# Performance work log

Hardware: AMD Instinct MI355X
Metric: run time of the kernel (lower is better)

The kernel has to match this reference:

```python
import jax, jax.numpy as jnp
import numpy as np

RADIUS = 0.3
NSAMPLE = 64
GROUPS = 8
GN_EPS = 1e-5
B, N = 8, 2048


def safe_norm(x, axis=-1, keepdims=False):
    # norm that matches sqrt exactly for nonzero inputs and returns 0 (not nan-grad) at 0
    ss = jnp.sum(x * x, axis=axis, keepdims=keepdims)
    zero = ss < 1e-20
    n = jnp.sqrt(jnp.where(zero, 1.0, ss))
    return jnp.where(zero, 0.0, n)


def angle(v1, v2):
    cross = jnp.cross(v1, v2)
    cn = jnp.sum(cross * cross, axis=-1)
    dot = jnp.sum(v1 * v2, axis=-1)
    deg = (cn < 1e-20) & (jnp.abs(dot) < 1e-12)
    cn_s = jnp.where(cn < 1e-20, 0.0, jnp.sqrt(jnp.where(cn < 1e-20, 1.0, cn)))
    ang = jnp.arctan2(cn_s, jnp.where(deg, 1.0, dot))
    return jnp.where(deg, 0.0, ang)  # torch atan2(0,0) = 0


def group_norm(x, gamma, beta):
    # x: [B, C, ...]; GroupNorm(8, C) over (C/8, spatial) per group
    b, c = x.shape[0], x.shape[1]
    xg = x.reshape(b, GROUPS, c // GROUPS, -1)
    mean = jnp.mean(xg, axis=(2, 3), keepdims=True)
    var = jnp.mean((xg - mean) ** 2, axis=(2, 3), keepdims=True)
    xn = ((xg - mean) * jax.lax.rsqrt(var + GN_EPS)).reshape(x.shape)
    bshape = (1, c) + (1,) * (x.ndim - 2)
    return xn * gamma.reshape(bshape) + beta.reshape(bshape)


def conv2d_1x1(x, w, b):  # x [B,Ci,S,N] -> [B,Co,S,N]
    return jnp.einsum('oc,bcsn->bosn', w, x) + b[None, :, None, None]


def conv1d_1x1(x, w, b):  # x [B,Ci,N] -> [B,Co,N]
    return jnp.einsum('oc,bcn->bon', w, x) + b[None, :, None]


def sample_and_group(xyz, normals):
    # npoint=-1: every point is a cluster center. Ball query within RADIUS, NSAMPLE neighbors.
    n = xyz.shape[1]
    sqr = jnp.sum((xyz[:, :, None, :] - xyz[:, None, :, :]) ** 2, axis=-1)  # [B,N,N]
    idx = jnp.broadcast_to(jnp.arange(n), sqr.shape)
    idx = jnp.where(sqr > RADIUS ** 2, n, idx)
    idx = jnp.sort(idx, axis=-1)[:, :, :NSAMPLE]            # first NSAMPLE in-radius (by index)
    idx = jnp.where(idx == n, idx[:, :, :1], idx)           # pad misses with first hit
    gather = jax.vmap(lambda pts, i: pts[i])                # per-batch gather
    g_xyz = gather(xyz, idx)                                # [B,N,ns,3]
    g_nr = gather(normals, idx)
    d = g_xyz - xyz[:, :, None, :]                          # dxyz [B,N,ns,3]
    nr = normals[:, :, None, :]
    ppf = jnp.stack([angle(nr, d), angle(g_nr, d), angle(nr, g_nr), safe_norm(d)], axis=-1)
    return d, ppf


def reference(xyz, normals,
              pre_w1, pre_b1, pre_g1, pre_be1,
              pre_w2, pre_b2, pre_g2, pre_be2,
              pre_w3, pre_b3, pre_g3, pre_be3,
              post_w1, post_b1, post_g1, post_be1,
              post_w2, post_b2, post_g2, post_be2,
              post_w3, post_b3):
    d, ppf = sample_and_group(xyz, normals)
    b, n = xyz.shape[0], xyz.shape[1]
    x_exp = jnp.broadcast_to(xyz[:, :, None, :], (b, n, NSAMPLE, 3))
    fused = jnp.concatenate([x_exp, d, ppf], axis=-1)       # features sorted: xyz, dxyz, ppf -> 10
    x = jnp.transpose(fused, (0, 3, 2, 1))                  # [B,10,ns,N]
    x = jax.nn.relu(group_norm(conv2d_1x1(x, pre_w1, pre_b1), pre_g1, pre_be1))
    x = jax.nn.relu(group_norm(conv2d_1x1(x, pre_w2, pre_b2), pre_g2, pre_be2))
    x = jax.nn.relu(group_norm(conv2d_1x1(x, pre_w3, pre_b3), pre_g3, pre_be3))
    pooled = jnp.max(x, axis=2)                             # max over neighbors -> [B,192,N]
    y = jax.nn.relu(group_norm(conv1d_1x1(pooled, post_w1, post_b1), post_g1, post_be1))
    y = jax.nn.relu(group_norm(conv1d_1x1(y, post_w2, post_b2), post_g2, post_be2))
    y = conv1d_1x1(y, post_w3, post_b3)
    feat = jnp.transpose(y, (0, 2, 1))                      # [B,N,96]
    return feat / safe_norm(feat, keepdims=True)


def setup_inputs() -> dict:
    key = jax.random.key(0)
    ks = jax.random.split(key, 16)
    emb2 = 192
    w = lambda k, o, i: 0.1 * jax.random.normal(k, (o, i), dtype=jnp.float32)
    bvec = lambda k, o: 0.1 * jax.random.normal(k, (o,), dtype=jnp.float32)
    return {
        'xyz': jax.random.uniform(ks[0], (B, N, 3), dtype=jnp.float32),
        'normals': jax.random.normal(ks[1], (B, N, 3), dtype=jnp.float32),
        'pre_w1': w(ks[2], 96, 10), 'pre_b1': bvec(ks[3], 96),
        'pre_g1': jnp.ones((96,), jnp.float32), 'pre_be1': jnp.zeros((96,), jnp.float32),
        'pre_w2': w(ks[4], 96, 96), 'pre_b2': bvec(ks[5], 96),
        'pre_g2': jnp.ones((96,), jnp.float32), 'pre_be2': jnp.zeros((96,), jnp.float32),
        'pre_w3': w(ks[6], emb2, 96), 'pre_b3': bvec(ks[7], emb2),
        'pre_g3': jnp.ones((emb2,), jnp.float32), 'pre_be3': jnp.zeros((emb2,), jnp.float32),
        'post_w1': w(ks[8], emb2, emb2), 'post_b1': bvec(ks[9], emb2),
        'post_g1': jnp.ones((emb2,), jnp.float32), 'post_be1': jnp.zeros((emb2,), jnp.float32),
        'post_w2': w(ks[10], 96, emb2), 'post_b2': bvec(ks[11], 96),
        'post_g2': jnp.ones((96,), jnp.float32), 'post_be2': jnp.zeros((96,), jnp.float32),
        'post_w3': w(ks[12], 96, 96), 'post_b3': bvec(ks[13], 96),
    }
```

## Files before the change

kernel.cpp:

```cpp
#include <hip/hip_runtime.h>
#include <math.h>

#define NPTS 2048
#define PPB  131072

typedef __attribute__((ext_vector_type(8))) short bf8_t;
typedef __attribute__((ext_vector_type(4))) float f4_t;

__device__ __forceinline__ unsigned short f2bf(float x) {
  unsigned u = __float_as_uint(x);
  u += 0x7FFFu + ((u >> 16) & 1u);
  return (unsigned short)(u >> 16);
}
__device__ __forceinline__ float bf2f(unsigned short h) {
  return __uint_as_float(((unsigned)h) << 16);
}
__device__ __forceinline__ unsigned cvt_pk_bf16(float a, float b) {
  unsigned r;
  asm("v_cvt_pk_bf16_f32 %0, %1, %2" : "=v"(r) : "v"(a), "v"(b));
  return r;
}
__device__ __forceinline__ void pack_h8(const float (&a)[8], bf8_t& h) {
  unsigned u[4];
#pragma unroll
  for (int i = 0; i < 4; ++i) u[i] = cvt_pk_bf16(a[2 * i], a[2 * i + 1]);
  h = *(const bf8_t*)u;
}

__device__ __forceinline__ float angle_f(float ax, float ay, float az,
                                         float bx, float by, float bz) {
  float cx = ay * bz - az * by;
  float cy = az * bx - ax * bz;
  float cz = ax * by - ay * bx;
  float cn = cx * cx + cy * cy + cz * cz;
  float dt = ax * bx + ay * by + az * bz;
  bool  sml = cn < 1e-20f;
  bool  deg = sml && (fabsf(dt) < 1e-12f);
  float cns = sml ? 0.0f : sqrtf(cn);
  float ang = atan2f(cns, dt);
  return deg ? 0.0f : ang;
}

__global__ __launch_bounds__(256) void k_wprep(
    const float* __restrict__ w1, const float* __restrict__ w2,
    const float* __restrict__ w3, const float* __restrict__ w4,
    const float* __restrict__ w5,
    unsigned short* __restrict__ wh1, unsigned short* __restrict__ wh2,
    unsigned short* __restrict__ wh3, unsigned short* __restrict__ wh4,
    unsigned short* __restrict__ wh5) {
  int t = blockIdx.x * 256 + threadIdx.x;
  if (t < 3072) {
    int i = t & 7, lane = (t >> 3) & 63, nt = t >> 9;
    int k = ((lane >> 4) << 3) + i;
    int n = nt * 16 + (lane & 15);
    wh1[t] = (k < 10) ? f2bf(w1[n * 10 + k]) : (unsigned short)0;
  } else if (t < 12288) {
    int f = t - 3072;
    int i = f & 7, lane = (f >> 3) & 63, r = f >> 9, nt = r % 6, ks = r / 6;
    int k = ks * 32 + ((lane >> 4) << 3) + i;
    int n = nt * 16 + (lane & 15);
    wh2[f] = f2bf(w2[n * 96 + k]);
  } else if (t < 30720) {
    int f = t - 12288;
    int i = f & 7, lane = (f >> 3) & 63, r = f >> 9, nt = r % 12, ks = r / 12;
    int k = ks * 32 + ((lane >> 4) << 3) + i;
    int n = nt * 16 + (lane & 15);
    wh3[f] = f2bf(w3[n * 96 + k]);
  } else if (t < 67584) {
    int f = t - 30720;
    int i = f & 7, lane = (f >> 3) & 63, r = f >> 9, nt = r % 12, ks = r / 12;
    int k = ks * 32 + ((lane >> 4) << 3) + i;
    int n = nt * 16 + (lane & 15);
    wh4[f] = f2bf(w4[n * 192 + k]);
  } else if (t < 86016) {
    int f = t - 67584;
    int i = f & 7, lane = (f >> 3) & 63, r = f >> 9, nt = r % 6, ks = r / 6;
    int k = ks * 32 + ((lane >> 4) << 3) + i;
    int n = nt * 16 + (lane & 15);
    wh5[f] = f2bf(w5[n * 192 + k]);
  }
}

__global__ __launch_bounds__(256) void k_feat(
    const float* __restrict__ xyz, const float* __restrict__ nrm,
    const float* __restrict__ w1, const float* __restrict__ b1,
    unsigned short* __restrict__ fused, float* __restrict__ st) {
  const int wid = threadIdx.x >> 6, lane = threadIdx.x & 63;
  const int b = blockIdx.x >> 9;
  const int n = ((blockIdx.x & 511) << 2) + wid;
  const float* X  = xyz + (size_t)b * NPTS * 3;
  const float* NR = nrm + (size_t)b * NPTS * 3;
  __shared__ int   lst[4][64];
  __shared__ float red[16];

  const float xi0 = X[n * 3 + 0], xi1 = X[n * 3 + 1], xi2 = X[n * 3 + 2];

  int cnt = 0;
  for (int jb = 0; jb < NPTS; jb += 64) {
    int   j  = jb + lane;
    float dx = __fsub_rn(xi0, X[j * 3 + 0]);
    float dy = __fsub_rn(xi1, X[j * 3 + 1]);
    float dz = __fsub_rn(xi2, X[j * 3 + 2]);
    float sq = __fadd_rn(__fadd_rn(__fmul_rn(dx, dx), __fmul_rn(dy, dy)),
                         __fmul_rn(dz, dz));
    bool act = (sq <= 0.09f);
    unsigned long long m = __ballot(act);
    int pos = cnt + __popcll(m & ((1ull << lane) - 1ull));
    if (act && pos < 64) lst[wid][pos] = j;
    cnt += __popcll(m);
    if (cnt >= 64) break;
  }
  __syncthreads();

  const int j = lst[wid][(lane < cnt) ? lane : 0];

  const float gx = X[j * 3 + 0],  gy = X[j * 3 + 1],  gz = X[j * 3 + 2];
  const float gnx = NR[j * 3 + 0], gny = NR[j * 3 + 1], gnz = NR[j * 3 + 2];
  const float nix = NR[n * 3 + 0], niy = NR[n * 3 + 1], niz = NR[n * 3 + 2];
  const float dx = gx - xi0, dy = gy - xi1, dz = gz - xi2;

  float f[10];
  f[0] = xi0; f[1] = xi1; f[2] = xi2;
  f[3] = dx;  f[4] = dy;  f[5] = dz;
  f[6] = angle_f(nix, niy, niz, dx, dy, dz);
  f[7] = angle_f(gnx, gny, gnz, dx, dy, dz);
  f[8] = angle_f(nix, niy, niz, gnx, gny, gnz);
  float ss = dx * dx + dy * dy + dz * dz;
  f[9] = (ss < 1e-20f) ? 0.0f : sqrtf(ss);

  size_t base = (size_t)b * 10 * PPB + (size_t)n * 64 + lane;
#pragma unroll
  for (int c = 0; c < 10; ++c) fused[base + (size_t)c * PPB] = f2bf(f[c]);

  float sg[8], qg[8];
#pragma unroll
  for (int g = 0; g < 8; ++g) {
    float s = 0.f, q = 0.f;
#pragma unroll
    for (int t2 = 0; t2 < 12; ++t2) {
      const int o = g * 12 + t2;
      float a = b1[o];
#pragma unroll
      for (int c = 0; c < 10; ++c) a += w1[o * 10 + c] * f[c];
      s += a; q += a * a;
    }
    sg[g] = s; qg[g] = q;
  }
#pragma unroll
  for (int g = 0; g < 8; ++g) {
#pragma unroll
    for (int off = 32; off; off >>= 1) {
      sg[g] += __shfl_xor(sg[g], off);
      qg[g] += __shfl_xor(qg[g], off);
    }
  }
  if (threadIdx.x < 16) red[threadIdx.x] = 0.f;
  __syncthreads();
  if (lane == 0) {
#pragma unroll
    for (int g = 0; g < 8; ++g) {
      atomicAdd(&red[2 * g + 0], sg[g]);
      atomicAdd(&red[2 * g + 1], qg[g]);
    }
  }
  __syncthreads();
  if (threadIdx.x < 16) atomicAdd(&st[b * 16 + threadIdx.x], red[threadIdx.x]);
}

#define GRAM_TILE(i, MT, NT) \
  acc[i] = __builtin_amdgcn_mfma_f32_16x16x32_bf16(fh##MT, fh##NT, acc[i], 0, 0, 0);
#define GRAM_LD(T) \
  bf8_t fh##T = *(const bf8_t*)&x1h[T * 16 + l15][ko];
#define GRAM_OUT(i, MT, NT) do { \
  _Pragma("unroll") \
  for (int r = 0; r < 4; ++r) \
    atomicAdd(&Gb[(MT * 16 + q * 4 + r) * 112 + NT * 16 + l15], acc[i][r]); \
} while (0)

__global__ __launch_bounds__(256) void k_gram(
    const unsigned short* __restrict__ fused, const unsigned short* __restrict__ wh1,
    const float* __restrict__ b1, const float* __restrict__ st1g,
    const float* __restrict__ g1, const float* __restrict__ be1,
    float* __restrict__ G) {
  __shared__ unsigned short x1h[112][72];
  __shared__ unsigned short x0bf[64][40];
  __shared__ float A1s[96], B1s[96], b1s[96];
  const int t = threadIdx.x, lane = t & 63, w = t >> 6;
  const int l15 = lane & 15, q = lane >> 4;
  const int b = blockIdx.x >> 6;
  const int blk = blockIdx.x & 63;

  if (t < 96) {
    int g = t / 12;
    float s = st1g[b * 16 + 2 * g], qq = st1g[b * 16 + 2 * g + 1];
    float mean = s * (1.0f / 1572864.0f);
    float var  = qq * (1.0f / 1572864.0f) - mean * mean;
    float r    = 1.0f / sqrtf(var + 1e-5f);
    float a    = g1[t] * r;
    A1s[t] = a; B1s[t] = be1[t] - mean * a; b1s[t] = b1[t];
  }
  for (int idx = t; idx < 16 * 72; idx += 256) {
    int ch = 96 + idx / 72, rr = idx % 72;
    x1h[ch][rr] = (ch == 96) ? (unsigned short)0x3F80 : (unsigned short)0;
  }
  __syncthreads();

  f4_t acc[7];
#pragma unroll
  for (int i = 0; i < 7; ++i) acc[i] = (f4_t){0.f, 0.f, 0.f, 0.f};

  for (int pt = 0; pt < 32; ++pt) {
    int n = blk * 32 + pt;
    size_t fb = (size_t)b * 10 * PPB + (size_t)n * 64;
    __syncthreads();
    for (int idx = t; idx < 64 * 11; idx += 256) {
      int R = idx / 11, u = 5 + idx % 11;
      *(unsigned*)&x0bf[R][u * 2] = 0u;
    }
    for (int idx = t; idx < 640; idx += 256) {
      int c = idx >> 6, s = idx & 63;
      x0bf[s][c] = fused[fb + (size_t)c * PPB + s];
    }
    __syncthreads();
    {
      bf8_t af0 = *(const bf8_t*)&x0bf[w * 16 + l15][q * 8];
#pragma unroll
      for (int nt = 0; nt < 6; ++nt) {
        f4_t a1c = (f4_t){0.f, 0.f, 0.f, 0.f};
        bf8_t bh = *(const bf8_t*)(wh1 + (((nt << 6) + lane) << 3));
        a1c = __builtin_amdgcn_mfma_f32_16x16x32_bf16(af0, bh, a1c, 0, 0, 0);
        const int ch = nt * 16 + l15;
        const float A = A1s[ch], Bb = B1s[ch], bi = b1s[ch];
#pragma unroll
        for (int r = 0; r < 4; ++r) {
          float x = A * (a1c[r] + bi) + Bb;
          x1h[ch][w * 16 + q * 4 + r] = f2bf(x > 0.f ? x : 0.f);
        }
      }
    }
    __syncthreads();
#pragma unroll
    for (int ksr = 0; ksr < 2; ++ksr) {
      const int ko = ksr * 32 + q * 8;
      GRAM_LD(0) GRAM_LD(1) GRAM_LD(2) GRAM_LD(3) GRAM_LD(4) GRAM_LD(5) GRAM_LD(6)
      if (w == 0) {
        GRAM_TILE(0, 0, 0); GRAM_TILE(1, 0, 1); GRAM_TILE(2, 0, 2);
        GRAM_TILE(3, 0, 3); GRAM_TILE(4, 0, 4); GRAM_TILE(5, 0, 5); GRAM_TILE(6, 0, 6);
      } else if (w == 1) {
        GRAM_TILE(0, 1, 1); GRAM_TILE(1, 1, 2); GRAM_TILE(2, 1, 3);
        GRAM_TILE(3, 1, 4); GRAM_TILE(4, 1, 5); GRAM_TILE(5, 1, 6); GRAM_TILE(6, 2, 2);
      } else if (w == 2) {
        GRAM_TILE(0, 2, 3); GRAM_TILE(1, 2, 4); GRAM_TILE(2, 2, 5);
        GRAM_TILE(3, 2, 6); GRAM_TILE(4, 3, 3); GRAM_TILE(5, 3, 4); GRAM_TILE(6, 3, 5);
      } else {
        GRAM_TILE(0, 3, 6); GRAM_TILE(1, 4, 4); GRAM_TILE(2, 4, 5);
        GRAM_TILE(3, 4, 6); GRAM_TILE(4, 5, 5); GRAM_TILE(5, 5, 6); GRAM_TILE(6, 6, 6);
      }
    }
  }
  float* Gb = G + (size_t)b * 12544;
  if (w == 0) {
    GRAM_OUT(0, 0, 0); GRAM_OUT(1, 0, 1); GRAM_OUT(2, 0, 2);
    GRAM_OUT(3, 0, 3); GRAM_OUT(4, 0, 4); GRAM_OUT(5, 0, 5); GRAM_OUT(6, 0, 6);
  } else if (w == 1) {
    GRAM_OUT(0, 1, 1); GRAM_OUT(1, 1, 2); GRAM_OUT(2, 1, 3);
    GRAM_OUT(3, 1, 4); GRAM_OUT(4, 1, 5); GRAM_OUT(5, 1, 6); GRAM_OUT(6, 2, 2);
  } else if (w == 2) {
    GRAM_OUT(0, 2, 3); GRAM_OUT(1, 2, 4); GRAM_OUT(2, 2, 5);
    GRAM_OUT(3, 2, 6); GRAM_OUT(4, 3, 3); GRAM_OUT(5, 3, 4); GRAM_OUT(6, 3, 5);
  } else {
    GRAM_OUT(0, 3, 6); GRAM_OUT(1, 4, 4); GRAM_OUT(2, 4, 5);
    GRAM_OUT(3, 4, 6); GRAM_OUT(4, 5, 5); GRAM_OUT(5, 5, 6); GRAM_OUT(6, 6, 6);
  }
}

__global__ void k_fin2(const float* __restrict__ G, const float* __restrict__ w2,
                       const float* __restrict__ b2, const float* __restrict__ gm,
                       const float* __restrict__ bt, float* __restrict__ A2,
                       float* __restrict__ B2) {
  __shared__ float Gs[96][97];
  __shared__ float s1s[96], cs[96], cq[96];
  __shared__ float qp[96][4];
  __shared__ float gsum[8][2];
  const int b = blockIdx.x, t = threadIdx.x;
  const int ch = t % 96, p = t / 96;
  for (int idx = t; idx < 9216; idx += 384) {
    int i = idx / 96, j = idx - i * 96;
    Gs[i][j] = ((i >> 4) <= (j >> 4)) ? G[b * 12544 + i * 112 + j]
                                      : G[b * 12544 + j * 112 + i];
  }
  if (t < 96) s1s[t] = G[b * 12544 + t * 112 + 96];
  __syncthreads();
  float wrow[96];
#pragma unroll
  for (int k = 0; k < 96; ++k) wrow[k] = w2[ch * 96 + k];
  float part = 0.f;
  for (int i = p * 24; i < p * 24 + 24; ++i) {
    float gi = 0.f;
#pragma unroll
    for (int jj = 0; jj < 96; ++jj) gi += Gs[i][jj] * wrow[jj];
    part += wrow[i] * gi;
  }
  qp[ch][p] = part;
  __syncthreads();
  if (t < 96) {
    float ds = 0.f;
#pragma unroll
    for (int k = 0; k < 96; ++k) ds += wrow[k] * s1s[k];
    float qf = qp[t][0] + qp[t][1] + qp[t][2] + qp[t][3];
    const float P = 131072.0f;
    cs[t] = ds + P * b2[t];
    cq[t] = qf + 2.0f * b2[t] * ds + P * b2[t] * b2[t];
  }
  __syncthreads();
  if (t < 8) {
    float s = 0.f, qq = 0.f;
    for (int k = 0; k < 12; ++k) { s += cs[t * 12 + k]; qq += cq[t * 12 + k]; }
    gsum[t][0] = s; gsum[t][1] = qq;
  }
  __syncthreads();
  if (t < 96) {
    int g = t / 12;
    float mean = gsum[g][0] * (1.0f / 1572864.0f);
    float var  = gsum[g][1] * (1.0f / 1572864.0f) - mean * mean;
    float r    = 1.0f / sqrtf(var + 1e-5f);
    float a    = gm[t] * r;
    A2[b * 96 + t] = a;
    B2[b * 96 + t] = bt[t] - mean * a;
  }
}

__global__ __launch_bounds__(256, 2) void k_main(
    const unsigned short* __restrict__ fused, const float* __restrict__ b1,
    const float* __restrict__ st1g, const float* __restrict__ g1,
    const float* __restrict__ be1, const unsigned short* __restrict__ wh1,
    const unsigned short* __restrict__ wh2, const float* __restrict__ b2,
    const float* __restrict__ A2, const float* __restrict__ B2,
    const unsigned short* __restrict__ wh3, const float* __restrict__ b3,
    float* __restrict__ zmx, float* __restrict__ zmn, float* __restrict__ st) {
  __shared__ unsigned short x0bf[260][40];
  __shared__ float b1s[96], A1s[96], B1s[96], b2s[96], A2s[96], B2s[96], b3s[192];
  __shared__ float bbr[4][16][35];
  __shared__ float pmx[4][192], pmn[4][192];
  __shared__ float red[16];

  const int t = threadIdx.x, lane = t & 63, w = t >> 6;
  const int l15 = lane & 15, q = lane >> 4;
  const int b = blockIdx.x >> 9;
  const int n0 = (blockIdx.x & 511) << 2;

  {
    size_t fb = (size_t)b * 10 * PPB + (size_t)n0 * 64;
    for (int idx = t; idx < 256 * 11; idx += 256) {
      int R = idx / 11, u = 5 + idx % 11;
      *(unsigned*)&x0bf[R][u * 2] = 0u;
    }
    for (int idx = t; idx < 2560; idx += 256) {
      int c = idx >> 8, R = idx & 255;
      x0bf[R][c] = fused[fb + (size_t)c * PPB + R];
    }
    if (t < 96) {
      b1s[t] = b1[t];
      b2s[t] = b2[t];  A2s[t] = A2[b * 96 + t];  B2s[t] = B2[b * 96 + t];
      int g = t / 12;
      float s = st1g[b * 16 + 2 * g], qq = st1g[b * 16 + 2 * g + 1];
      float mean = s * (1.0f / 1572864.0f);
      float var  = qq * (1.0f / 1572864.0f) - mean * mean;
      float r    = 1.0f / sqrtf(var + 1e-5f);
      float a    = g1[t] * r;
      A1s[t] = a; B1s[t] = be1[t] - mean * a;
    }
    if (t < 192) b3s[t] = b3[t];
    if (t < 16) red[t] = 0.f;
  }
  __syncthreads();

  bf8_t af0[4];
#pragma unroll
  for (int rt = 0; rt < 4; ++rt)
    af0[rt] = *(const bf8_t*)&x0bf[w * 64 + rt * 16 + l15][q * 8];

  bf8_t a1[4][3];
#pragma unroll
  for (int k2 = 0; k2 < 3; ++k2) {
    f4_t acc1[2][4];
#pragma unroll
    for (int half = 0; half < 2; ++half)
#pragma unroll
      for (int rt = 0; rt < 4; ++rt) acc1[half][rt] = (f4_t){0.f, 0.f, 0.f, 0.f};
#pragma unroll
    for (int half = 0; half < 2; ++half) {
      const int nt = k2 * 2 + half;
      bf8_t bh = *(const bf8_t*)(wh1 + (((nt << 6) + lane) << 3));
#pragma unroll
      for (int rt = 0; rt < 4; ++rt)
        acc1[half][rt] = __builtin_amdgcn_mfma_f32_16x16x32_bf16(af0[rt], bh, acc1[half][rt], 0, 0, 0);
    }
#pragma unroll
    for (int rt = 0; rt < 4; ++rt) {
#pragma unroll
      for (int half = 0; half < 2; ++half) {
        const int nt = k2 * 2 + half;
        const int ch = nt * 16 + l15;
        const float a1c = A1s[ch], bg = B1s[ch], bi = b1s[ch];
#pragma unroll
        for (int r = 0; r < 4; ++r) {
          float x = a1c * (acc1[half][rt][r] + bi) + bg;
          bbr[w][q * 4 + r][half * 16 + l15] = x > 0.f ? x : 0.f;
        }
      }
      __builtin_amdgcn_wave_barrier();
      {
        float vv[8];
#pragma unroll
        for (int i = 0; i < 8; ++i) vv[i] = bbr[w][l15][q * 8 + i];
        pack_h8(vv, a1[rt][k2]);
      }
      __builtin_amdgcn_wave_barrier();
    }
  }

  bf8_t A3[4][3];
#pragma unroll
  for (int k2 = 0; k2 < 3; ++k2) {
    f4_t acc2[2][4];
#pragma unroll
    for (int half = 0; half < 2; ++half)
#pragma unroll
      for (int rt = 0; rt < 4; ++rt) acc2[half][rt] = (f4_t){0.f, 0.f, 0.f, 0.f};
#pragma unroll
    for (int half = 0; half < 2; ++half) {
      const int nt = k2 * 2 + half;
#pragma unroll
      for (int ks = 0; ks < 3; ++ks) {
        bf8_t bh = *(const bf8_t*)(wh2 + ((((ks * 6 + nt) << 6) + lane) << 3));
#pragma unroll
        for (int rt = 0; rt < 4; ++rt)
          acc2[half][rt] = __builtin_amdgcn_mfma_f32_16x16x32_bf16(a1[rt][ks], bh, acc2[half][rt], 0, 0, 0);
      }
    }
#pragma unroll
    for (int rt = 0; rt < 4; ++rt) {
#pragma unroll
      for (int half = 0; half < 2; ++half) {
        const int nt = k2 * 2 + half;
        const int ch = nt * 16 + l15;
        const float a2 = A2s[ch], bg = B2s[ch], bi = b2s[ch];
#pragma unroll
        for (int r = 0; r < 4; ++r) {
          float x = a2 * (acc2[half][rt][r] + bi) + bg;
          bbr[w][q * 4 + r][half * 16 + l15] = x > 0.f ? x : 0.f;
        }
      }
      __builtin_amdgcn_wave_barrier();
      {
        float vv[8];
#pragma unroll
        for (int i = 0; i < 8; ++i) vv[i] = bbr[w][l15][q * 8 + i];
        pack_h8(vv, A3[rt][k2]);
      }
      __builtin_amdgcn_wave_barrier();
    }
  }

  float sg[8], qg[8];
#pragma unroll
  for (int g = 0; g < 8; ++g) { sg[g] = 0.f; qg[g] = 0.f; }
#pragma unroll
  for (int nt = 0; nt < 12; ++nt) {
    f4_t ac[4];
#pragma unroll
    for (int rt = 0; rt < 4; ++rt) ac[rt] = (f4_t){0.f, 0.f, 0.f, 0.f};
#pragma unroll
    for (int ks = 0; ks < 3; ++ks) {
      bf8_t bh = *(const bf8_t*)(wh3 + ((((ks * 12 + nt) << 6) + lane) << 3));
#pragma unroll
      for (int rt = 0; rt < 4; ++rt)
        ac[rt] = __builtin_amdgcn_mfma_f32_16x16x32_bf16(A3[rt][ks], bh, ac[rt], 0, 0, 0);
    }
    int ch = nt * 16 + l15;
    float bi = b3s[ch];
    float s = 0.f, qq = 0.f, mx = -3.4e38f, mn = 3.4e38f;
#pragma unroll
    for (int rt = 0; rt < 4; ++rt) {
#pragma unroll
      for (int r = 0; r < 4; ++r) {
        float v = ac[rt][r] + bi;
        s += v; qq += v * v;
        mx = fmaxf(mx, v); mn = fminf(mn, v);
      }
    }
    mx = fmaxf(mx, __shfl_xor(mx, 16)); mx = fmaxf(mx, __shfl_xor(mx, 32));
    mn = fminf(mn, __shfl_xor(mn, 16)); mn = fminf(mn, __shfl_xor(mn, 32));
    if (lane < 16) { pmx[w][nt * 16 + lane] = mx; pmn[w][nt * 16 + lane] = mn; }
    const int g0 = (nt * 16) / 24;
    const int g1i = (nt * 16 + 15) / 24;
    if (g0 == g1i) {
      sg[g0] += s; qg[g0] += qq;
    } else {
      const int cut = g1i * 24 - nt * 16;
      if (l15 < cut) { sg[g0] += s; qg[g0] += qq; }
      else           { sg[g1i] += s; qg[g1i] += qq; }
    }
  }

#pragma unroll
  for (int g = 0; g < 8; ++g) {
#pragma unroll
    for (int off = 1; off < 64; off <<= 1) {
      sg[g] += __shfl_xor(sg[g], off);
      qg[g] += __shfl_xor(qg[g], off);
    }
  }
  if (lane == 0) {
#pragma unroll
    for (int g = 0; g < 8; ++g) {
      atomicAdd(&red[2 * g + 0], sg[g]);
      atomicAdd(&red[2 * g + 1], qg[g]);
    }
  }
  {
    int n = n0 + w;
    size_t ob = ((size_t)(b * NPTS + n)) * 192;
    for (int i = lane; i < 192; i += 64) {
      zmx[ob + i] = pmx[w][i];
      zmn[ob + i] = pmn[w][i];
    }
  }
  __syncthreads();
  if (t < 16) atomicAdd(&st[b * 16 + t], red[t]);
}

__global__ __launch_bounds__(128) void k_post1(
    const float* __restrict__ zmx, const float* __restrict__ zmn,
    const float* __restrict__ st3, const float* __restrict__ g3,
    const float* __restrict__ be3, const unsigned short* __restrict__ wh4,
    const float* __restrict__ b4, unsigned short* __restrict__ z4bf,
    float* __restrict__ st4) {
  __shared__ unsigned short ybf[32][200];
  __shared__ float A3s[192], B3s[192], b4s[192];
  __shared__ float red[16];
  const int t = threadIdx.x, lane = t & 63, w = t >> 6;
  const int l15 = lane & 15, q = lane >> 4;
  const int p0 = blockIdx.x << 5;
  const int b = p0 >> 11;

  for (int c = t; c < 192; c += 128) {
    int g = c / 24;
    float s = st3[b * 16 + 2 * g], qq = st3[b * 16 + 2 * g + 1];
    float mean = s * (1.0f / 3145728.0f);
    float var  = qq * (1.0f / 3145728.0f) - mean * mean;
    float r    = 1.0f / sqrtf(var + 1e-5f);
    float a    = g3[c] * r;
    A3s[c] = a; B3s[c] = be3[c] - mean * a; b4s[c] = b4[c];
  }
  if (t < 16) red[t] = 0.f;
  __syncthreads();

  for (int idx = t; idx < 32 * 192; idx += 128) {
    int ptl = idx / 192, ch = idx - ptl * 192;
    float A = A3s[ch];
    const float* src = (A > 0.f) ? zmx : zmn;
    float x = A * src[(size_t)(p0 + ptl) * 192 + ch] + B3s[ch];
    ybf[ptl][ch] = f2bf(x > 0.f ? x : 0.f);
  }
  __syncthreads();

  bf8_t af[6];
#pragma unroll
  for (int ks = 0; ks < 6; ++ks)
    af[ks] = *(const bf8_t*)&ybf[w * 16 + l15][ks * 32 + q * 8];
  __syncthreads();

  float sg[8], qg[8];
#pragma unroll
  for (int g = 0; g < 8; ++g) { sg[g] = 0.f; qg[g] = 0.f; }
#pragma unroll
  for (int nt = 0; nt < 12; ++nt) {
    f4_t ac = (f4_t){0.f, 0.f, 0.f, 0.f};
#pragma unroll
    for (int ks = 0; ks < 6; ++ks) {
      bf8_t bh = *(const bf8_t*)(wh4 + ((((ks * 12 + nt) << 6) + lane) << 3));
      ac = __builtin_amdgcn_mfma_f32_16x16x32_bf16(af[ks], bh, ac, 0, 0, 0);
    }
    int ch = nt * 16 + l15;
    float bi = b4s[ch];
    float s = 0.f, qq = 0.f;
#pragma unroll
    for (int r = 0; r < 4; ++r) {
      float v = ac[r] + bi;
      s += v; qq += v * v;
      ybf[w * 16 + q * 4 + r][ch] = f2bf(v);
    }
    const int g0 = (nt * 16) / 24;
    const int g1i = (nt * 16 + 15) / 24;
    if (g0 == g1i) {
      sg[g0] += s; qg[g0] += qq;
    } else {
      const int cut = g1i * 24 - nt * 16;
      if (l15 < cut) { sg[g0] += s; qg[g0] += qq; }
      else           { sg[g1i] += s; qg[g1i] += qq; }
    }
  }
#pragma unroll
  for (int g = 0; g < 8; ++g) {
#pragma unroll
    for (int off = 1; off < 64; off <<= 1) {
      sg[g] += __shfl_xor(sg[g], off);
      qg[g] += __shfl_xor(qg[g], off);
    }
  }
  if (lane == 0) {
#pragma unroll
    for (int g = 0; g < 8; ++g) {
      atomicAdd(&red[2 * g + 0], sg[g]);
      atomicAdd(&red[2 * g + 1], qg[g]);
    }
  }
  __syncthreads();
  unsigned* z4u = (unsigned*)z4bf;
  for (int idx = t; idx < 32 * 96; idx += 128) {
    int ptl = idx / 96, pr = idx - ptl * 96;
    z4u[(size_t)(p0 + ptl) * 96 + pr] = *(const unsigned*)&ybf[ptl][pr * 2];
  }
  if (t < 16) atomicAdd(&st4[b * 16 + t], red[t]);
}

__global__ __launch_bounds__(128) void k_post2(
    const unsigned short* __restrict__ z4bf, const float* __restrict__ st4,
    const float* __restrict__ g4, const float* __restrict__ be4,
    const unsigned short* __restrict__ wh5, const float* __restrict__ b5,
    unsigned short* __restrict__ z5bf, float* __restrict__ st5) {
  __shared__ unsigned short ybf[32][200];
  __shared__ float A4s[192], B4s[192], b5s[96];
  __shared__ float red[16];
  const int t = threadIdx.x, lane = t & 63, w = t >> 6;
  const int l15 = lane & 15, q = lane >> 4;
  const int p0 = blockIdx.x << 5;
  const int b = p0 >> 11;

  for (int c = t; c < 192; c += 128) {
    int g = c / 24;
    float s = st4[b * 16 + 2 * g], qq = st4[b * 16 + 2 * g + 1];
    float mean = s * (1.0f / 49152.0f);
    float var  = qq * (1.0f / 49152.0f) - mean * mean;
    float r    = 1.0f / sqrtf(var + 1e-5f);
    float a    = g4[c] * r;
    A4s[c] = a; B4s[c] = be4[c] - mean * a;
  }
  if (t < 96) b5s[t] = b5[t];
  if (t < 16) red[t] = 0.f;
  __syncthreads();

  const unsigned* z4u = (const unsigned*)z4bf;
  for (int idx = t; idx < 32 * 96; idx += 128) {
    int ptl = idx / 96, pr = idx - ptl * 96;
    unsigned v = z4u[(size_t)(p0 + ptl) * 96 + pr];
    int ch = pr * 2;
    float x0 = A4s[ch] * bf2f((unsigned short)(v & 0xffff)) + B4s[ch];
    float x1 = A4s[ch + 1] * bf2f((unsigned short)(v >> 16)) + B4s[ch + 1];
    x0 = x0 > 0.f ? x0 : 0.f;
    x1 = x1 > 0.f ? x1 : 0.f;
    *(unsigned*)&ybf[ptl][ch] = cvt_pk_bf16(x0, x1);
  }
  __syncthreads();

  bf8_t af[6];
#pragma unroll
  for (int ks = 0; ks < 6; ++ks)
    af[ks] = *(const bf8_t*)&ybf[w * 16 + l15][ks * 32 + q * 8];
  __syncthreads();

  float sg[8], qg[8];
#pragma unroll
  for (int g = 0; g < 8; ++g) { sg[g] = 0.f; qg[g] = 0.f; }
#pragma unroll
  for (int nt = 0; nt < 6; ++nt) {
    f4_t ac = (f4_t){0.f, 0.f, 0.f, 0.f};
#pragma unroll
    for (int ks = 0; ks < 6; ++ks) {
      bf8_t bh = *(const bf8_t*)(wh5 + ((((ks * 6 + nt) << 6) + lane) << 3));
      ac = __builtin_amdgcn_mfma_f32_16x16x32_bf16(af[ks], bh, ac, 0, 0, 0);
    }
    int ch = nt * 16 + l15;
    float bi = b5s[ch];
    float s = 0.f, qq = 0.f;
#pragma unroll
    for (int r = 0; r < 4; ++r) {
      float v = ac[r] + bi;
      s += v; qq += v * v;
      ybf[w * 16 + q * 4 + r][ch] = f2bf(v);
    }
    const int g0 = (nt * 16) / 12;
    const int g1i = (nt * 16 + 15) / 12;
    const int cut = g1i * 12 - nt * 16;
    if (l15 < cut) { sg[g0] += s; qg[g0] += qq; }
    else           { sg[g1i] += s; qg[g1i] += qq; }
  }
#pragma unroll
  for (int g = 0; g < 8; ++g) {
#pragma unroll
    for (int off = 1; off < 64; off <<= 1) {
      sg[g] += __shfl_xor(sg[g], off);
      qg[g] += __shfl_xor(qg[g], off);
    }
  }
  if (lane == 0) {
#pragma unroll
    for (int g = 0; g < 8; ++g) {
      atomicAdd(&red[2 * g + 0], sg[g]);
      atomicAdd(&red[2 * g + 1], qg[g]);
    }
  }
  __syncthreads();
  unsigned* z5u = (unsigned*)z5bf;
  for (int idx = t; idx < 32 * 48; idx += 128) {
    int ptl = idx / 48, pr = idx - ptl * 48;
    z5u[(size_t)(p0 + ptl) * 48 + pr] = *(const unsigned*)&ybf[ptl][pr * 2];
  }
  if (t < 16) atomicAdd(&st5[b * 16 + t], red[t]);
}

__global__ __launch_bounds__(128) void k_post3(
    const unsigned short* __restrict__ z5bf, const float* __restrict__ st5,
    const float* __restrict__ g5, const float* __restrict__ be5,
    const float* __restrict__ w6, const float* __restrict__ b6,
    float* __restrict__ out) {
  __shared__ float y[32][100];
  __shared__ float w6s[96][96];
  __shared__ float A5s[96], B5s[96], b6s[96];
  __shared__ float inv[32];
  const int t = threadIdx.x;
  const int ptl = t & 31, grp = t >> 5;
  const int p0 = blockIdx.x << 5;
  const int b = p0 >> 11;

  if (t < 96) {
    int g = t / 12;
    float s = st5[b * 16 + 2 * g], qq = st5[b * 16 + 2 * g + 1];
    float mean = s * (1.0f / 24576.0f);
    float var  = qq * (1.0f / 24576.0f) - mean * mean;
    float r    = 1.0f / sqrtf(var + 1e-5f);
    float a    = g5[t] * r;
    A5s[t] = a; B5s[t] = be5[t] - mean * a; b6s[t] = b6[t];
  }
  for (int idx = t; idx < 9216; idx += 128)
    w6s[idx / 96][idx % 96] = w6[idx];
  __syncthreads();

  const unsigned* z5u = (const unsigned*)z5bf;
  for (int idx = t; idx < 32 * 48; idx += 128) {
    int pl = idx / 48, pr = idx - pl * 48;
    unsigned v = z5u[(size_t)(p0 + pl) * 48 + pr];
    int ch = pr * 2;
    float x0 = A5s[ch] * bf2f((unsigned short)(v & 0xffff)) + B5s[ch];
    float x1 = A5s[ch + 1] * bf2f((unsigned short)(v >> 16)) + B5s[ch + 1];
    y[pl][ch]     = x0 > 0.f ? x0 : 0.f;
    y[pl][ch + 1] = x1 > 0.f ? x1 : 0.f;
  }
  __syncthreads();

  const int ob = grp * 24;
  float z[24];
#pragma unroll
  for (int kb = 0; kb < 3; ++kb) {
    float a[8];
#pragma unroll
    for (int k = 0; k < 8; ++k) a[k] = b6s[ob + kb * 8 + k];
    for (int c4 = 0; c4 < 24; ++c4) {
      float4 xv = *(const float4*)&y[ptl][c4 * 4];
#pragma unroll
      for (int k = 0; k < 8; ++k) {
        const float* wr = &w6s[ob + kb * 8 + k][c4 * 4];
        a[k] += wr[0] * xv.x + wr[1] * xv.y + wr[2] * xv.z + wr[3] * xv.w;
      }
    }
#pragma unroll
    for (int k = 0; k < 8; ++k) z[kb * 8 + k] = a[k];
  }
  __syncthreads();
#pragma unroll
  for (int jj = 0; jj < 24; ++jj) y[ptl][ob + jj] = z[jj];
  __syncthreads();
  if (t < 32) {
    float ss = 0.f;
#pragma unroll
    for (int c = 0; c < 96; ++c) { float v = y[t][c]; ss += v * v; }
    float nf = (ss < 1e-20f) ? 0.0f : sqrtf(ss);
    inv[t] = 1.0f / nf;
  }
  __syncthreads();
  for (int idx = t; idx < 32 * 96; idx += 128) {
    int pl = idx / 96, ch = idx - pl * 96;
    out[(size_t)(p0 + pl) * 96 + ch] = y[pl][ch] * inv[pl];
  }
}

extern "C" void kernel_launch(void* const* d_in, const int* in_sizes, int n_in,
                              void* d_out, int out_size, void* d_ws, size_t ws_size,
                              hipStream_t stream) {
  (void)in_sizes; (void)n_in; (void)out_size; (void)ws_size;
  const float* xyz = (const float*)d_in[0];
  const float* nrm = (const float*)d_in[1];
  const float* w1 = (const float*)d_in[2];  const float* b1 = (const float*)d_in[3];
  const float* g1 = (const float*)d_in[4];  const float* be1 = (const float*)d_in[5];
  const float* w2 = (const float*)d_in[6];  const float* b2 = (const float*)d_in[7];
  const float* g2 = (const float*)d_in[8];  const float* be2 = (const float*)d_in[9];
  const float* w3 = (const float*)d_in[10]; const float* b3 = (const float*)d_in[11];
  const float* g3 = (const float*)d_in[12]; const float* be3 = (const float*)d_in[13];
  const float* w4 = (const float*)d_in[14]; const float* b4 = (const float*)d_in[15];
  const float* g4 = (const float*)d_in[16]; const float* be4 = (const float*)d_in[17];
  const float* w5 = (const float*)d_in[18]; const float* b5 = (const float*)d_in[19];
  const float* g5 = (const float*)d_in[20]; const float* be5 = (const float*)d_in[21];
  const float* w6 = (const float*)d_in[22]; const float* b6 = (const float*)d_in[23];

  float* ws = (float*)d_ws;
  unsigned short* fused = (unsigned short*)ws;
  float* zmx = ws + 5242880;
  float* zmn = zmx + 3145728;
  float* st1 = zmn + 3145728;
  float* st3 = st1 + 128;
  float* st4 = st3 + 128;
  float* st5 = st4 + 128;
  float* A2 = st5 + 128;  float* B2 = A2 + 768;
  float* wbuf = B2 + 768;
  unsigned short* wh1 = (unsigned short*)wbuf;
  unsigned short* wh2 = wh1 + 3072;
  unsigned short* wh3 = wh2 + 9216;
  unsigned short* wh4 = wh3 + 18432;
  unsigned short* wh5 = wh4 + 36864;
  float* G = wbuf + 43008;
  unsigned short* z4bf = (unsigned short*)(G + 100352);
  unsigned short* z5bf = z4bf + 3145728;

  hipMemsetAsync(st1, 0, 4 * 128 * sizeof(float), stream);
  hipMemsetAsync(G, 0, 8 * 12544 * sizeof(float), stream);

  k_wprep <<<336, 256, 0, stream>>>(w1, w2, w3, w4, w5, wh1, wh2, wh3, wh4, wh5);
  k_feat  <<<4096, 256, 0, stream>>>(xyz, nrm, w1, b1, fused, st1);
  k_gram  <<<512, 256, 0, stream>>>(fused, wh1, b1, st1, g1, be1, G);
  k_fin2  <<<8, 384, 0, stream>>>(G, w2, b2, g2, be2, A2, B2);
  k_main  <<<4096, 256, 0, stream>>>(fused, b1, st1, g1, be1, wh1, wh2, b2, A2, B2,
                                     wh3, b3, zmx, zmn, st3);
  k_post1 <<<512, 128, 0, stream>>>(zmx, zmn, st3, g3, be3, wh4, b4, z4bf, st4);
  k_post2 <<<512, 128, 0, stream>>>(z4bf, st4, g4, be4, wh5, b5, z5bf, st5);
  k_post3 <<<512, 128, 0, stream>>>(z5bf, st5, g5, be5, w6, b6, (float*)d_out);
}
```

Before: 456.4 us.

## Batch two points per gram iteration and store max/min pooled features as bf16

The gram kernel now stages two points per loop iteration in double-sized shared buffers, halving the number of barrier-separated iterations. Separately, the per-point max/min pooled outputs of k_main are written as bf16 instead of fp32, and k_post1 reads them as bf16. This halves that intermediate's write and read traffic but rounds the pooled values before group-norm, which may affect accuracy. The larger shared-memory footprint in k_gram could also lower occupancy.

After: 446.0 us. 1.02x faster.

```diff
diff --git a/kernel.cpp b/kernel.cpp
--- a/kernel.cpp
+++ b/kernel.cpp
@@ -170,7 +170,7 @@
 #define GRAM_TILE(i, MT, NT) \
   acc[i] = __builtin_amdgcn_mfma_f32_16x16x32_bf16(fh##MT, fh##NT, acc[i], 0, 0, 0);
 #define GRAM_LD(T) \
-  bf8_t fh##T = *(const bf8_t*)&x1h[T * 16 + l15][ko];
+  bf8_t fh##T = *(const bf8_t*)&x1h[pp][T * 16 + l15][ko];
 #define GRAM_OUT(i, MT, NT) do { \
   _Pragma("unroll") \
   for (int r = 0; r < 4; ++r) \
@@ -182,8 +182,8 @@
     const float* __restrict__ b1, const float* __restrict__ st1g,
     const float* __restrict__ g1, const float* __restrict__ be1,
     float* __restrict__ G) {
-  __shared__ unsigned short x1h[112][72];
-  __shared__ unsigned short x0bf[64][40];
+  __shared__ unsigned short x1h[2][112][72];
+  __shared__ unsigned short x0bf[128][40];
   __shared__ float A1s[96], B1s[96], b1s[96];
   const int t = threadIdx.x, lane = t & 63, w = t >> 6;
   const int l15 = lane & 15, q = lane >> 4;
@@ -199,9 +199,10 @@
     float a    = g1[t] * r;
     A1s[t] = a; B1s[t] = be1[t] - mean * a; b1s[t] = b1[t];
   }
-  for (int idx = t; idx < 16 * 72; idx += 256) {
-    int ch = 96 + idx / 72, rr = idx % 72;
-    x1h[ch][rr] = (ch == 96) ? (unsigned short)0x3F80 : (unsigned short)0;
+  for (int idx = t; idx < 2 * 16 * 72; idx += 256) {
+    int pp = idx / (16 * 72), rem = idx % (16 * 72);
+    int ch = 96 + rem / 72, rr = rem % 72;
+    x1h[pp][ch][rr] = (ch == 96) ? (unsigned short)0x3F80 : (unsigned short)0;
   }
   __syncthreads();
 
@@ -209,21 +210,22 @@
 #pragma unroll
   for (int i = 0; i < 7; ++i) acc[i] = (f4_t){0.f, 0.f, 0.f, 0.f};
 
-  for (int pt = 0; pt < 32; ++pt) {
-    int n = blk * 32 + pt;
+  for (int it = 0; it < 16; ++it) {
+    int n = blk * 32 + it * 2;
     size_t fb = (size_t)b * 10 * PPB + (size_t)n * 64;
     __syncthreads();
-    for (int idx = t; idx < 64 * 11; idx += 256) {
+    for (int idx = t; idx < 128 * 11; idx += 256) {
       int R = idx / 11, u = 5 + idx % 11;
       *(unsigned*)&x0bf[R][u * 2] = 0u;
     }
-    for (int idx = t; idx < 640; idx += 256) {
-      int c = idx >> 6, s = idx & 63;
+    for (int idx = t; idx < 1280; idx += 256) {
+      int c = idx >> 7, s = idx & 127;
       x0bf[s][c] = fused[fb + (size_t)c * PPB + s];
     }
     __syncthreads();
-    {
-      bf8_t af0 = *(const bf8_t*)&x0bf[w * 16 + l15][q * 8];
+#pragma unroll
+    for (int pp = 0; pp < 2; ++pp) {
+      bf8_t af0 = *(const bf8_t*)&x0bf[pp * 64 + w * 16 + l15][q * 8];
 #pragma unroll
       for (int nt = 0; nt < 6; ++nt) {
         f4_t a1c = (f4_t){0.f, 0.f, 0.f, 0.f};
@@ -234,27 +236,30 @@
 #pragma unroll
         for (int r = 0; r < 4; ++r) {
           float x = A * (a1c[r] + bi) + Bb;
-          x1h[ch][w * 16 + q * 4 + r] = f2bf(x > 0.f ? x : 0.f);
+          x1h[pp][ch][w * 16 + q * 4 + r] = f2bf(x > 0.f ? x : 0.f);
         }
       }
     }
     __syncthreads();
 #pragma unroll
-    for (int ksr = 0; ksr < 2; ++ksr) {
-      const int ko = ksr * 32 + q * 8;
-      GRAM_LD(0) GRAM_LD(1) GRAM_LD(2) GRAM_LD(3) GRAM_LD(4) GRAM_LD(5) GRAM_LD(6)
-      if (w == 0) {
-        GRAM_TILE(0, 0, 0); GRAM_TILE(1, 0, 1); GRAM_TILE(2, 0, 2);
-        GRAM_TILE(3, 0, 3); GRAM_TILE(4, 0, 4); GRAM_TILE(5, 0, 5); GRAM_TILE(6, 0, 6);
-      } else if (w == 1) {
-        GRAM_TILE(0, 1, 1); GRAM_TILE(1, 1, 2); GRAM_TILE(2, 1, 3);
-        GRAM_TILE(3, 1, 4); GRAM_TILE(4, 1, 5); GRAM_TILE(5, 1, 6); GRAM_TILE(6, 2, 2);
-      } else if (w == 2) {
-        GRAM_TILE(0, 2, 3); GRAM_TILE(1, 2, 4); GRAM_TILE(2, 2, 5);
-        GRAM_TILE(3, 2, 6); GRAM_TILE(4, 3, 3); GRAM_TILE(5, 3, 4); GRAM_TILE(6, 3, 5);
-      } else {
-        GRAM_TILE(0, 3, 6); GRAM_TILE(1, 4, 4); GRAM_TILE(2, 4, 5);
-        GRAM_TILE(3, 4, 6); GRAM_TILE(4, 5, 5); GRAM_TILE(5, 5, 6); GRAM_TILE(6, 6, 6);
+    for (int pp = 0; pp < 2; ++pp) {
+#pragma unroll
+      for (int ksr = 0; ksr < 2; ++ksr) {
+        const int ko = ksr * 32 + q * 8;
+        GRAM_LD(0) GRAM_LD(1) GRAM_LD(2) GRAM_LD(3) GRAM_LD(4) GRAM_LD(5) GRAM_LD(6)
+        if (w == 0) {
+          GRAM_TILE(0, 0, 0); GRAM_TILE(1, 0, 1); GRAM_TILE(2, 0, 2);
+          GRAM_TILE(3, 0, 3); GRAM_TILE(4, 0, 4); GRAM_TILE(5, 0, 5); GRAM_TILE(6, 0, 6);
+        } else if (w == 1) {
+          GRAM_TILE(0, 1, 1); GRAM_TILE(1, 1, 2); GRAM_TILE(2, 1, 3);
+          GRAM_TILE(3, 1, 4); GRAM_TILE(4, 1, 5); GRAM_TILE(5, 1, 6); GRAM_TILE(6, 2, 2);
+        } else if (w == 2) {
+          GRAM_TILE(0, 2, 3); GRAM_TILE(1, 2, 4); GRAM_TILE(2, 2, 5);
+          GRAM_TILE(3, 2, 6); GRAM_TILE(4, 3, 3); GRAM_TILE(5, 3, 4); GRAM_TILE(6, 3, 5);
+        } else {
+          GRAM_TILE(0, 3, 6); GRAM_TILE(1, 4, 4); GRAM_TILE(2, 4, 5);
+          GRAM_TILE(3, 4, 6); GRAM_TILE(4, 5, 5); GRAM_TILE(5, 5, 6); GRAM_TILE(6, 6, 6);
+        }
       }
     }
   }
@@ -337,7 +342,8 @@
     const unsigned short* __restrict__ wh2, const float* __restrict__ b2,
     const float* __restrict__ A2, const float* __restrict__ B2,
     const unsigned short* __restrict__ wh3, const float* __restrict__ b3,
-    float* __restrict__ zmx, float* __restrict__ zmn, float* __restrict__ st) {
+    unsigned short* __restrict__ zmx, unsigned short* __restrict__ zmn,
+    float* __restrict__ st) {
   __shared__ unsigned short x0bf[260][40];
   __shared__ float b1s[96], A1s[96], B1s[96], b2s[96], A2s[96], B2s[96], b3s[192];
   __shared__ float bbr[4][16][35];
@@ -523,8 +529,8 @@
     int n = n0 + w;
     size_t ob = ((size_t)(b * NPTS + n)) * 192;
     for (int i = lane; i < 192; i += 64) {
-      zmx[ob + i] = pmx[w][i];
-      zmn[ob + i] = pmn[w][i];
+      zmx[ob + i] = f2bf(pmx[w][i]);
+      zmn[ob + i] = f2bf(pmn[w][i]);
     }
   }
   __syncthreads();
@@ -532,7 +538,7 @@
 }
 
 __global__ __launch_bounds__(128) void k_post1(
-    const float* __restrict__ zmx, const float* __restrict__ zmn,
+    const unsigned short* __restrict__ zmx, const unsigned short* __restrict__ zmn,
     const float* __restrict__ st3, const float* __restrict__ g3,
     const float* __restrict__ be3, const unsigned short* __restrict__ wh4,
     const float* __restrict__ b4, unsigned short* __restrict__ z4bf,
@@ -560,8 +566,8 @@
   for (int idx = t; idx < 32 * 192; idx += 128) {
     int ptl = idx / 192, ch = idx - ptl * 192;
     float A = A3s[ch];
-    const float* src = (A > 0.f) ? zmx : zmn;
-    float x = A * src[(size_t)(p0 + ptl) * 192 + ch] + B3s[ch];
+    const unsigned short* src = (A > 0.f) ? zmx : zmn;
+    float x = A * bf2f(src[(size_t)(p0 + ptl) * 192 + ch]) + B3s[ch];
     ybf[ptl][ch] = f2bf(x > 0.f ? x : 0.f);
   }
   __syncthreads();
@@ -816,9 +822,9 @@
 
   float* ws = (float*)d_ws;
   unsigned short* fused = (unsigned short*)ws;
-  float* zmx = ws + 5242880;
-  float* zmn = zmx + 3145728;
-  float* st1 = zmn + 3145728;
+  unsigned short* zmxbf = (unsigned short*)(ws + 5242880);
+  unsigned short* zmnbf = zmxbf + 3145728;
+  float* st1 = ws + 5242880 + 3145728;
   float* st3 = st1 + 128;
   float* st4 = st3 + 128;
   float* st5 = st4 + 128;
@@ -841,8 +847,8 @@
   k_gram  <<<512, 256, 0, stream>>>(fused, wh1, b1, st1, g1, be1, G);
   k_fin2  <<<8, 384, 0, stream>>>(G, w2, b2, g2, be2, A2, B2);
   k_main  <<<4096, 256, 0, stream>>>(fused, b1, st1, g1, be1, wh1, wh2, b2, A2, B2,
-                                     wh3, b3, zmx, zmn, st3);
-  k_post1 <<<512, 128, 0, stream>>>(zmx, zmn, st3, g3, be3, wh4, b4, z4bf, st4);
+                                     wh3, b3, zmxbf, zmnbf, st3);
+  k_post1 <<<512, 128, 0, stream>>>(zmxbf, zmnbf, st3, g3, be3, wh4, b4, z4bf, st4);
   k_post2 <<<512, 128, 0, stream>>>(z4bf, st4, g4, be4, wh5, b5, z5bf, st5);
   k_post3 <<<512, 128, 0, stream>>>(z5bf, st5, g5, be5, w6, b6, (float*)d_out);
 }
```
